# Kernel optimization log

Measured on AMD Instinct MI355X. Metric: run time of the kernel, lower is better.

## Reference

```python
import jax, jax.numpy as jnp
import numpy as np

N = 20000
E = 320000
IN_F = 128
HEADS = 8
OUT_F = 32
NEG_SLOPE = 0.2


def setup_inputs() -> dict:
    key = jax.random.key(0)
    k = jax.random.split(key, 8)
    x = jax.random.normal(k[0], (N, IN_F), dtype=jnp.float32)
    edge_index = jax.random.randint(k[1], (2, E), 0, N, dtype=jnp.int32)
    # Linear weights stored torch-style: [out, in]
    scale = 1.0 / np.sqrt(IN_F)
    W = jax.random.normal(k[2], (HEADS * OUT_F, IN_F), dtype=jnp.float32) * scale
    W1 = jax.random.normal(k[3], (HEADS * OUT_F, IN_F), dtype=jnp.float32) * scale
    W2 = jax.random.normal(k[4], (HEADS * OUT_F, IN_F), dtype=jnp.float32) * scale
    att = jax.random.normal(k[5], (1, HEADS, OUT_F), dtype=jnp.float32) * 0.1
    bias = jnp.zeros((HEADS * OUT_F,), dtype=jnp.float32)
    return {"x": x, "edge_index": edge_index, "W": W, "W1": W1, "W2": W2,
            "att": att, "bias": bias}


def reference(x, edge_index, W, W1, W2, att, bias):
    n, heads, out_f = x.shape[0], att.shape[1], att.shape[2]
    src, dst = edge_index[0], edge_index[1]

    # Node projections: [N, H, F]
    h_src = (x @ W1.T).reshape(n, heads, out_f)
    h_dst = (x @ W2.T).reshape(n, heads, out_f)
    values = (x @ W.T).reshape(n, heads, out_f)

    # Edge-wise GATv2 logits: a^T LeakyReLU(W1 h_i + W2 h_j)  -> [E, H]
    att_input = jax.nn.leaky_relu(h_src[src] + h_dst[dst], negative_slope=NEG_SLOPE)
    logits = jnp.einsum('ehf,hf->eh', att_input, att[0])

    # Segment softmax over incoming edges of each dst node (stable).
    seg_max = jax.ops.segment_max(logits, dst, num_segments=n)  # [N, H]
    exp_l = jnp.exp(logits - seg_max[dst])
    denom = jax.ops.segment_sum(exp_l, dst, num_segments=n)     # [N, H]
    weights = exp_l / denom[dst]                                # [E, H]

    # Weighted aggregation of source values into dst nodes.
    weighted = weights[:, :, None] * values[src]                # [E, H, F]
    out = jax.ops.segment_sum(weighted, dst, num_segments=n)    # [N, H, F]

    out = out.reshape(n, heads * out_f) + bias
    return out
```

## Files before the change

### kernel.cpp

```cpp
#include <hip/hip_runtime.h>
#include <math.h>

#define NN 20000
#define EE 320000
#define KF 128
#define HO 256
#define CAP 96

typedef __attribute__((ext_vector_type(8))) short short8;
typedef __attribute__((ext_vector_type(4))) float f32x4;

static __device__ __forceinline__ unsigned short f2bf(float f) {
    union { float f; unsigned u; } v; v.f = f;
    unsigned u = v.u;
    u += 0x7fffu + ((u >> 16) & 1u);
    return (unsigned short)(u >> 16);
}
static __device__ __forceinline__ float bf2f(unsigned short b) {
    union { unsigned u; float f; } v; v.u = ((unsigned)b) << 16;
    return v.f;
}

__global__ __launch_bounds__(256, 2) void proj_kernel(
    const float* __restrict__ x, const float* __restrict__ W0,
    const float* __restrict__ W1, const float* __restrict__ W2,
    unsigned short* __restrict__ hv, unsigned short* __restrict__ hdst,
    int* __restrict__ cursor)
{
    const int m = blockIdx.y;
    const float* __restrict__ Wm = (m == 0) ? W0 : (m == 1) ? W1 : W2;
    unsigned short* __restrict__ dst = (m == 0) ? (hv + 256) : (m == 1) ? hv : hdst;
    const int stride = (m == 2) ? 256 : 512;

    if (m == 0 && blockIdx.x < 79) {
        int i = blockIdx.x * 256 + threadIdx.x;
        if (i < NN) cursor[i] = 0;
    }

    const int nb   = blockIdx.x * 128;
    const int w    = threadIdx.x >> 6;
    const int lane = threadIdx.x & 63;
    const int lr   = lane & 15;
    const int q    = lane >> 4;

    f32x4 acc[2][16];
#pragma unroll
    for (int mi = 0; mi < 2; ++mi)
#pragma unroll
        for (int nt = 0; nt < 16; ++nt) acc[mi][nt] = (f32x4){0.f, 0.f, 0.f, 0.f};

    const int r0 = nb + w * 32;

    for (int ks = 0; ks < 4; ++ks) {
        const int kcol = ks * 32 + q * 8;
        short8 a_f[2];
#pragma unroll
        for (int mi = 0; mi < 2; ++mi) {
            const int row = r0 + mi * 16 + lr;
            float4 xa = make_float4(0.f, 0.f, 0.f, 0.f), xb = xa;
            if (row < NN) {
                const float* xp = x + (size_t)row * KF + kcol;
                xa = *(const float4*)xp;
                xb = *(const float4*)(xp + 4);
            }
            a_f[mi][0] = (short)f2bf(xa.x); a_f[mi][1] = (short)f2bf(xa.y);
            a_f[mi][2] = (short)f2bf(xa.z); a_f[mi][3] = (short)f2bf(xa.w);
            a_f[mi][4] = (short)f2bf(xb.x); a_f[mi][5] = (short)f2bf(xb.y);
            a_f[mi][6] = (short)f2bf(xb.z); a_f[mi][7] = (short)f2bf(xb.w);
        }
#pragma unroll
        for (int nt = 0; nt < 16; ++nt) {
            const float* wp = Wm + (size_t)(nt * 16 + lr) * KF + kcol;
            float4 wa = *(const float4*)wp;
            float4 wb = *(const float4*)(wp + 4);
            short8 b_f;
            b_f[0] = (short)f2bf(wa.x); b_f[1] = (short)f2bf(wa.y);
            b_f[2] = (short)f2bf(wa.z); b_f[3] = (short)f2bf(wa.w);
            b_f[4] = (short)f2bf(wb.x); b_f[5] = (short)f2bf(wb.y);
            b_f[6] = (short)f2bf(wb.z); b_f[7] = (short)f2bf(wb.w);
#pragma unroll
            for (int mi = 0; mi < 2; ++mi)
                acc[mi][nt] = __builtin_amdgcn_mfma_f32_16x16x32_bf16(a_f[mi], b_f, acc[mi][nt], 0, 0, 0);
        }
    }

#pragma unroll
    for (int mi = 0; mi < 2; ++mi) {
        const int rbase = r0 + mi * 16 + q * 4;
#pragma unroll
        for (int r = 0; r < 4; ++r) {
            const int row = rbase + r;
            if (row < NN) {
#pragma unroll
                for (int nt = 0; nt < 16; ++nt)
                    dst[(size_t)row * stride + nt * 16 + lr] = f2bf(acc[mi][nt][r]);
            }
        }
    }
}

__global__ void scatter_kernel(const int* __restrict__ ei, int* __restrict__ cursor,
                               int* __restrict__ csr_src) {
    int e = blockIdx.x * blockDim.x + threadIdx.x;
    if (e < EE) {
        int s = ei[e];
        int d = ei[EE + e];
        int pos = atomicAdd(&cursor[d], 1);
        if (pos < CAP) csr_src[d * CAP + pos] = s;
    }
}

__global__ __launch_bounds__(128) void gat_kernel(
    const unsigned short* __restrict__ hv, const unsigned short* __restrict__ hdst,
    const float* __restrict__ att, const float* __restrict__ bias,
    const int* __restrict__ cursor, const int* __restrict__ csr_src,
    float* __restrict__ out)
{
    const int w    = threadIdx.x >> 6;
    const int d    = blockIdx.x * 2 + w;
    const int lane = threadIdx.x & 63;
    const int col  = lane * 4;

    const float4 a4 = *(const float4*)(att + col);
    const float4 b4 = *(const float4*)(bias + col);
    const ushort4 hd4 = *(const ushort4*)(hdst + (size_t)d * HO + col);
    const float hd0 = bf2f(hd4.x), hd1 = bf2f(hd4.y), hd2 = bf2f(hd4.z), hd3 = bf2f(hd4.w);

    int deg = cursor[d];
    if (deg > CAP) deg = CAP;

    int sreg = (lane < deg) ? csr_src[d * CAP + lane] : 0;

    float l = 0.f;
    float o0 = 0.f, o1 = 0.f, o2 = 0.f, o3 = 0.f;

#define EDGE_CALC(HV, VV)                                                     \
    {                                                                         \
        float z0 = bf2f(HV.x) + hd0, z1 = bf2f(HV.y) + hd1;                   \
        float z2 = bf2f(HV.z) + hd2, z3 = bf2f(HV.w) + hd3;                   \
        z0 = fmaxf(z0, 0.2f * z0); z1 = fmaxf(z1, 0.2f * z1);                 \
        z2 = fmaxf(z2, 0.2f * z2); z3 = fmaxf(z3, 0.2f * z3);                 \
        float p = fmaf(a4.x, z0, a4.y * z1) + fmaf(a4.z, z2, a4.w * z3);      \
        p += __shfl_xor(p, 1); p += __shfl_xor(p, 2); p += __shfl_xor(p, 4);  \
        const float e = __expf(p);                                            \
        l += e;                                                               \
        o0 = fmaf(e, bf2f(VV.x), o0);                                         \
        o1 = fmaf(e, bf2f(VV.y), o1);                                         \
        o2 = fmaf(e, bf2f(VV.z), o2);                                         \
        o3 = fmaf(e, bf2f(VV.w), o3);                                         \
    }

    const int nfast = (deg < 64) ? deg : 64;
    int i = 0;
    for (; i + 4 <= nfast; i += 4) {
        const int s0 = __shfl(sreg, i);
        const int s1 = __shfl(sreg, i + 1);
        const int s2 = __shfl(sreg, i + 2);
        const int s3 = __shfl(sreg, i + 3);
        const unsigned short* p0 = hv + (size_t)s0 * 512 + col;
        const unsigned short* p1 = hv + (size_t)s1 * 512 + col;
        const unsigned short* p2 = hv + (size_t)s2 * 512 + col;
        const unsigned short* p3 = hv + (size_t)s3 * 512 + col;
        const ushort4 hv0 = *(const ushort4*)p0;
        const ushort4 vv0 = *(const ushort4*)(p0 + 256);
        const ushort4 hv1 = *(const ushort4*)p1;
        const ushort4 vv1 = *(const ushort4*)(p1 + 256);
        const ushort4 hv2 = *(const ushort4*)p2;
        const ushort4 vv2 = *(const ushort4*)(p2 + 256);
        const ushort4 hv3 = *(const ushort4*)p3;
        const ushort4 vv3 = *(const ushort4*)(p3 + 256);
        EDGE_CALC(hv0, vv0);
        EDGE_CALC(hv1, vv1);
        EDGE_CALC(hv2, vv2);
        EDGE_CALC(hv3, vv3);
    }
    for (; i < nfast; ++i) {
        const int s0 = __shfl(sreg, i);
        const unsigned short* p0 = hv + (size_t)s0 * 512 + col;
        const ushort4 hv0 = *(const ushort4*)p0;
        const ushort4 vv0 = *(const ushort4*)(p0 + 256);
        EDGE_CALC(hv0, vv0);
    }
    for (int j = 64; j < deg; ++j) {
        const int s0 = csr_src[d * CAP + j];
        const unsigned short* p0 = hv + (size_t)s0 * 512 + col;
        const ushort4 hv0 = *(const ushort4*)p0;
        const ushort4 vv0 = *(const ushort4*)(p0 + 256);
        EDGE_CALC(hv0, vv0);
    }
#undef EDGE_CALC

    const float inv = (deg > 0) ? 1.f / l : 0.f;
    float4 res;
    res.x = o0 * inv + b4.x;
    res.y = o1 * inv + b4.y;
    res.z = o2 * inv + b4.z;
    res.w = o3 * inv + b4.w;
    *(float4*)(out + (size_t)d * HO + col) = res;
}

extern "C" void kernel_launch(void* const* d_in, const int* in_sizes, int n_in,
                              void* d_out, int out_size, void* d_ws, size_t ws_size,
                              hipStream_t stream) {
    const float* x    = (const float*)d_in[0];
    const int*   ei   = (const int*)d_in[1];
    const float* W0   = (const float*)d_in[2];
    const float* W1   = (const float*)d_in[3];
    const float* W2   = (const float*)d_in[4];
    const float* att  = (const float*)d_in[5];
    const float* bias = (const float*)d_in[6];
    float* out = (float*)d_out;

    char* p = (char*)d_ws;
    unsigned short* hv   = (unsigned short*)p; p += (size_t)NN * 512 * 2;
    unsigned short* hdst = (unsigned short*)p; p += (size_t)NN * HO * 2;
    int* cursor  = (int*)p; p += (size_t)NN * sizeof(int);
    int* csr_src = (int*)p; p += (size_t)NN * CAP * sizeof(int);

    proj_kernel<<<dim3((NN + 127) / 128, 3), 256, 0, stream>>>(x, W0, W1, W2, hv, hdst, cursor);
    scatter_kernel<<<(EE + 255) / 256, 256, 0, stream>>>(ei, cursor, csr_src);
    gat_kernel<<<NN / 2, 128, 0, stream>>>(hv, hdst, att, bias, cursor, csr_src, out);
}
```

Baseline: 175.6 us.

## Pre-convert x and weights to bf16, stage projection outputs through LDS

Adds a prep kernel that converts x and the three weight matrices to bf16 once (and zeroes the cursor), so the projection GEMM loads packed bf16 fragments directly instead of converting fp32 on every load. The projection kernel now uses 64-row tiles with one M-tile per wave and higher occupancy. It writes results through shared memory so global stores are 16-byte row-contiguous rather than scattered 2-byte stores. This adds an extra kernel launch and a round trip for the bf16 copy of x through memory.

```diff
diff --git a/kernel.cpp b/kernel.cpp
--- a/kernel.cpp
+++ b/kernel.cpp
@@ -21,81 +21,31 @@
     return v.f;
 }
 
-__global__ __launch_bounds__(256, 2) void proj_kernel(
+__global__ __launch_bounds__(256) void prep_kernel(
     const float* __restrict__ x, const float* __restrict__ W0,
     const float* __restrict__ W1, const float* __restrict__ W2,
-    unsigned short* __restrict__ hv, unsigned short* __restrict__ hdst,
+    unsigned short* __restrict__ xb, unsigned short* __restrict__ wb,
     int* __restrict__ cursor)
 {
-    const int m = blockIdx.y;
-    const float* __restrict__ Wm = (m == 0) ? W0 : (m == 1) ? W1 : W2;
-    unsigned short* __restrict__ dst = (m == 0) ? (hv + 256) : (m == 1) ? hv : hdst;
-    const int stride = (m == 2) ? 256 : 512;
-
-    if (m == 0 && blockIdx.x < 79) {
-        int i = blockIdx.x * 256 + threadIdx.x;
+    const int b = blockIdx.x;
+    const int t = threadIdx.x;
+    if (b < 96) {
+        const int m = b >> 5;
+        const float* __restrict__ Wm = (m == 0) ? W0 : (m == 1) ? W1 : W2;
+        int idx = (b & 31) * 1024 + t * 4;
+        float4 v = *(const float4*)(Wm + idx);
+        ushort4 o;
+        o.x = f2bf(v.x); o.y = f2bf(v.y); o.z = f2bf(v.z); o.w = f2bf(v.w);
+        *(ushort4*)(wb + (size_t)m * 32768 + idx) = o;
+    } else if (b < 2596) {
+        size_t i = (size_t)(b - 96) * 1024 + t * 4;
+        float4 v = *(const float4*)(x + i);
+        ushort4 o;
+        o.x = f2bf(v.x); o.y = f2bf(v.y); o.z = f2bf(v.z); o.w = f2bf(v.w);
+        *(ushort4*)(xb + i) = o;
+    } else {
+        int i = (b - 2596) * 256 + t;
         if (i < NN) cursor[i] = 0;
-    }
-
-    const int nb   = blockIdx.x * 128;
-    const int w    = threadIdx.x >> 6;
-    const int lane = threadIdx.x & 63;
-    const int lr   = lane & 15;
-    const int q    = lane >> 4;
-
-    f32x4 acc[2][16];
-#pragma unroll
-    for (int mi = 0; mi < 2; ++mi)
-#pragma unroll
-        for (int nt = 0; nt < 16; ++nt) acc[mi][nt] = (f32x4){0.f, 0.f, 0.f, 0.f};
-
-    const int r0 = nb + w * 32;
-
-    for (int ks = 0; ks < 4; ++ks) {
-        const int kcol = ks * 32 + q * 8;
-        short8 a_f[2];
-#pragma unroll
-        for (int mi = 0; mi < 2; ++mi) {
-            const int row = r0 + mi * 16 + lr;
-            float4 xa = make_float4(0.f, 0.f, 0.f, 0.f), xb = xa;
-            if (row < NN) {
-                const float* xp = x + (size_t)row * KF + kcol;
-                xa = *(const float4*)xp;
-                xb = *(const float4*)(xp + 4);
-            }
-            a_f[mi][0] = (short)f2bf(xa.x); a_f[mi][1] = (short)f2bf(xa.y);
-            a_f[mi][2] = (short)f2bf(xa.z); a_f[mi][3] = (short)f2bf(xa.w);
-            a_f[mi][4] = (short)f2bf(xb.x); a_f[mi][5] = (short)f2bf(xb.y);
-            a_f[mi][6] = (short)f2bf(xb.z); a_f[mi][7] = (short)f2bf(xb.w);
-        }
-#pragma unroll
-        for (int nt = 0; nt < 16; ++nt) {
-            const float* wp = Wm + (size_t)(nt * 16 + lr) * KF + kcol;
-            float4 wa = *(const float4*)wp;
-            float4 wb = *(const float4*)(wp + 4);
-            short8 b_f;
-            b_f[0] = (short)f2bf(wa.x); b_f[1] = (short)f2bf(wa.y);
-            b_f[2] = (short)f2bf(wa.z); b_f[3] = (short)f2bf(wa.w);
-            b_f[4] = (short)f2bf(wb.x); b_f[5] = (short)f2bf(wb.y);
-            b_f[6] = (short)f2bf(wb.z); b_f[7] = (short)f2bf(wb.w);
-#pragma unroll
-            for (int mi = 0; mi < 2; ++mi)
-                acc[mi][nt] = __builtin_amdgcn_mfma_f32_16x16x32_bf16(a_f[mi], b_f, acc[mi][nt], 0, 0, 0);
-        }
-    }
-
-#pragma unroll
-    for (int mi = 0; mi < 2; ++mi) {
-        const int rbase = r0 + mi * 16 + q * 4;
-#pragma unroll
-        for (int r = 0; r < 4; ++r) {
-            const int row = rbase + r;
-            if (row < NN) {
-#pragma unroll
-                for (int nt = 0; nt < 16; ++nt)
-                    dst[(size_t)row * stride + nt * 16 + lr] = f2bf(acc[mi][nt][r]);
-            }
-        }
     }
 }
 
@@ -107,6 +57,60 @@
         int d = ei[EE + e];
         int pos = atomicAdd(&cursor[d], 1);
         if (pos < CAP) csr_src[d * CAP + pos] = s;
+    }
+}
+
+__global__ __launch_bounds__(256, 3) void proj_kernel(
+    const unsigned short* __restrict__ xb, const unsigned short* __restrict__ wb,
+    unsigned short* __restrict__ hv, unsigned short* __restrict__ hdst)
+{
+    __shared__ unsigned short lds[4][16][256];
+
+    const int m = blockIdx.y;
+    const unsigned short* __restrict__ Wm = wb + (size_t)m * 32768;
+    unsigned short* __restrict__ dst = (m == 0) ? (hv + 256) : (m == 1) ? hv : hdst;
+    const int stride = (m == 2) ? 256 : 512;
+
+    const int w    = threadIdx.x >> 6;
+    const int lane = threadIdx.x & 63;
+    const int lr   = lane & 15;
+    const int q    = lane >> 4;
+    const int r0   = blockIdx.x * 64 + w * 16;
+
+    f32x4 acc[16];
+#pragma unroll
+    for (int nt = 0; nt < 16; ++nt) acc[nt] = (f32x4){0.f, 0.f, 0.f, 0.f};
+
+#pragma unroll
+    for (int ks = 0; ks < 4; ++ks) {
+        const int kcol = ks * 32 + q * 8;
+        const int arow = r0 + lr;
+        short8 a_f = (short8){0,0,0,0,0,0,0,0};
+        if (arow < NN) a_f = *(const short8*)(xb + (size_t)arow * KF + kcol);
+#pragma unroll
+        for (int nt = 0; nt < 16; ++nt) {
+            short8 b_f = *(const short8*)(Wm + (size_t)(nt * 16 + lr) * KF + kcol);
+            acc[nt] = __builtin_amdgcn_mfma_f32_16x16x32_bf16(a_f, b_f, acc[nt], 0, 0, 0);
+        }
+    }
+
+#pragma unroll
+    for (int nt = 0; nt < 16; ++nt)
+#pragma unroll
+        for (int r = 0; r < 4; ++r)
+            lds[w][q * 4 + r][nt * 16 + lr] = f2bf(acc[nt][r]);
+    __syncthreads();
+
+    const int half = lane >> 5;
+    const int xoff = (lane & 31) * 8;
+#pragma unroll
+    for (int it = 0; it < 8; ++it) {
+        const int rl = it * 2 + half;
+        const int r  = r0 + rl;
+        if (r < NN) {
+            short8 v = *(const short8*)&lds[w][rl][xoff];
+            *(short8*)(dst + (size_t)r * stride + xoff) = v;
+        }
     }
 }
 
@@ -214,10 +218,13 @@
     char* p = (char*)d_ws;
     unsigned short* hv   = (unsigned short*)p; p += (size_t)NN * 512 * 2;
     unsigned short* hdst = (unsigned short*)p; p += (size_t)NN * HO * 2;
+    unsigned short* xb   = (unsigned short*)p; p += (size_t)NN * KF * 2;
+    unsigned short* wb   = (unsigned short*)p; p += (size_t)3 * 32768 * 2;
     int* cursor  = (int*)p; p += (size_t)NN * sizeof(int);
     int* csr_src = (int*)p; p += (size_t)NN * CAP * sizeof(int);
 
-    proj_kernel<<<dim3((NN + 127) / 128, 3), 256, 0, stream>>>(x, W0, W1, W2, hv, hdst, cursor);
+    prep_kernel<<<2675, 256, 0, stream>>>(x, W0, W1, W2, xb, wb, cursor);
     scatter_kernel<<<(EE + 255) / 256, 256, 0, stream>>>(ei, cursor, csr_src);
+    proj_kernel<<<dim3(313, 3), 256, 0, stream>>>(xb, wb, hv, hdst);
     gat_kernel<<<NN / 2, 128, 0, stream>>>(hv, hdst, att, bias, cursor, csr_src, out);
 }
```

New measurement: 176.2 us. Within noise of the previous version (+0.3%).
